# Performance work log

Measured on AMD Instinct MI355X. Metric: run time of the kernel, lower is better.

Reference implementation:

```python
import jax, jax.numpy as jnp
import numpy as np

DIM = 256
HEADS = 8
WIN = 8
HIDDEN = 1024
EPS = 1e-5

def _rel_pos_index(w):
    coords = np.stack(np.meshgrid(np.arange(w), np.arange(w), indexing='ij'))  # [2,w,w]
    cf = coords.reshape(2, -1)
    rel = cf[:, :, None] - cf[:, None, :]  # [2,N,N]
    rel = rel.transpose(1, 2, 0)
    rel[:, :, 0] += w - 1
    rel[:, :, 1] += w - 1
    rel[:, :, 0] *= 2 * w - 1
    return jnp.asarray(rel.sum(-1))  # [N,N] int

REL_IDX = _rel_pos_index(WIN)

def _layernorm(x, g, b):
    mu = jnp.mean(x, -1, keepdims=True)
    var = jnp.mean(jnp.square(x - mu), -1, keepdims=True)
    return (x - mu) * jax.lax.rsqrt(var + EPS) * g + b

def setup_inputs() -> dict:
    key = jax.random.key(0)
    ks = jax.random.split(key, 12)
    s = 0.02
    return {
        'x': jax.random.normal(ks[0], (16, 4096, 256), jnp.float32),
        'H': 64,
        'W': 64,
        'ln1_g': jnp.ones((DIM,), jnp.float32),
        'ln1_b': jnp.zeros((DIM,), jnp.float32),
        'qkv_w': jax.random.normal(ks[1], (DIM, 3 * DIM), jnp.float32) * s,
        'proj_w': jax.random.normal(ks[2], (DIM, DIM), jnp.float32) * s,
        'proj_b': jnp.zeros((DIM,), jnp.float32),
        'rel_bias_table': jax.random.normal(ks[3], ((2 * WIN - 1) ** 2, HEADS), jnp.float32) * s,
        'ln2_g': jnp.ones((DIM,), jnp.float32),
        'ln2_b': jnp.zeros((DIM,), jnp.float32),
        'fc1_w': jax.random.normal(ks[4], (DIM, HIDDEN), jnp.float32) * s,
        'fc1_b': jnp.zeros((HIDDEN,), jnp.float32),
        'fc2_w': jax.random.normal(ks[5], (HIDDEN, DIM), jnp.float32) * s,
        'fc2_b': jnp.zeros((DIM,), jnp.float32),
    }

def reference(x, H, W, ln1_g, ln1_b, qkv_w, proj_w, proj_b, rel_bias_table,
              ln2_g, ln2_b, fc1_w, fc1_b, fc2_w, fc2_b):
    B, L, C = x.shape
    w = WIN
    N = w * w
    head_dim = C // HEADS
    scale = head_dim ** -0.5

    shortcut = x
    h = _layernorm(x, ln1_g, ln1_b).reshape(B, H, W, C)
    # H, W chosen divisible by window_size -> pad_h = pad_w = 0 (faithful fast path)
    # window partition: [B*nW, N, C]
    h = h.reshape(B, H // w, w, W // w, w, C).transpose(0, 1, 3, 2, 4, 5)
    xw = h.reshape(-1, N, C)
    Bw = xw.shape[0]

    qkv = (xw @ qkv_w).reshape(Bw, N, 3, HEADS, head_dim)
    q = qkv[:, :, 0].transpose(0, 2, 1, 3) * scale  # [Bw,h,N,d]
    k = qkv[:, :, 1].transpose(0, 2, 1, 3)
    v = qkv[:, :, 2].transpose(0, 2, 1, 3)

    attn = jnp.einsum('bhnd,bhmd->bhnm', q, k)
    bias = rel_bias_table[REL_IDX.reshape(-1)].reshape(N, N, HEADS).transpose(2, 0, 1)
    attn = jax.nn.softmax(attn + bias[None], axis=-1)
    out = jnp.einsum('bhnm,bhmd->bhnd', attn, v).transpose(0, 2, 1, 3).reshape(Bw, N, C)
    out = out @ proj_w + proj_b

    # window reverse
    out = out.reshape(B, H // w, W // w, w, w, C).transpose(0, 1, 3, 2, 4, 5)
    out = out.reshape(B, L, C)

    x = shortcut + out
    h2 = _layernorm(x, ln2_g, ln2_b)
    mlp = jax.nn.gelu(h2 @ fc1_w + fc1_b, approximate=False) @ fc2_w + fc2_b
    return x + mlp
```

## Files before the change

### kernel.cpp

```cpp
#include <hip/hip_runtime.h>
#include <hip/hip_bf16.h>

typedef __attribute__((ext_vector_type(8))) short bf16x8;
typedef __attribute__((ext_vector_type(4))) float f32x4;

typedef __attribute__((address_space(3))) void LdsVoid;
typedef const __attribute__((address_space(1))) void GblVoid;

__device__ __forceinline__ void gload16(const void* g, void* l) {
  __builtin_amdgcn_global_load_lds((GblVoid*)g, (LdsVoid*)l, 16, 0, 0);
}

__device__ __forceinline__ unsigned short f2bf(float f) {
  union { float f; unsigned int u; } x; x.f = f;
  unsigned int r = (x.u + 0x7fffu + ((x.u >> 16) & 1u)) >> 16;
  return (unsigned short)r;
}

__global__ __launch_bounds__(256) void prep_w(
    const float* __restrict__ qw, const float* __restrict__ pw,
    const float* __restrict__ f1, const float* __restrict__ f2,
    unsigned short* __restrict__ out) {
  int idx = blockIdx.x * 256 + threadIdx.x;
  if (idx < 196608) { int n = idx >> 8, k = idx & 255; out[idx] = f2bf(qw[k * 768 + n]); return; }
  int i2 = idx - 196608;
  if (i2 < 65536) { int n = i2 >> 8, k = i2 & 255; out[idx] = f2bf(pw[k * 256 + n]); return; }
  int i3 = i2 - 65536;
  if (i3 < 262144) { int n = i3 >> 8, k = i3 & 255; out[idx] = f2bf(f1[k * 1024 + n]); return; }
  int i4 = i3 - 262144;
  { int n = i4 >> 10, k = i4 & 1023; out[idx] = f2bf(f2[k * 256 + n]); }
}

__global__ __launch_bounds__(256) void ln1_kernel(
    const float* __restrict__ x, const float* __restrict__ g, const float* __restrict__ b,
    unsigned short* __restrict__ xn) {
  int lane = threadIdx.x & 63, wid = threadIdx.x >> 6;
  size_t t = (size_t)blockIdx.x * 4 + wid;
  float4 v = ((const float4*)(x + t * 256))[lane];
  float s = v.x + v.y + v.z + v.w;
  #pragma unroll
  for (int m = 1; m < 64; m <<= 1) s += __shfl_xor(s, m);
  float mean = s * (1.0f / 256.0f);
  float dx = v.x - mean, dy = v.y - mean, dz = v.z - mean, dw = v.w - mean;
  float q = dx * dx + dy * dy + dz * dz + dw * dw;
  #pragma unroll
  for (int m = 1; m < 64; m <<= 1) q += __shfl_xor(q, m);
  float rstd = rsqrtf(q * (1.0f / 256.0f) + 1e-5f);
  float4 gg = ((const float4*)g)[lane];
  float4 bb = ((const float4*)b)[lane];
  unsigned int o0 = f2bf(dx * rstd * gg.x + bb.x) | ((unsigned int)f2bf(dy * rstd * gg.y + bb.y) << 16);
  unsigned int o1 = f2bf(dz * rstd * gg.z + bb.z) | ((unsigned int)f2bf(dw * rstd * gg.w + bb.w) << 16);
  int bI = (int)(t >> 12), rem = (int)t & 4095, y = rem >> 6, xc = rem & 63;
  size_t r = ((size_t)(bI * 64 + (y >> 3) * 8 + (xc >> 3))) * 64 + (y & 7) * 8 + (xc & 7);
  uint2 o; o.x = o0; o.y = o1;
  ((uint2*)(xn + r * 256))[lane] = o;
}

template <int EPI>
__global__ __launch_bounds__(256) void gemm_bt(
    const unsigned short* __restrict__ A, const unsigned short* __restrict__ Bt,
    unsigned short* __restrict__ outb, float* __restrict__ outf,
    const float* __restrict__ bias, const float* __restrict__ xres,
    int M, int N, int K) {
  __shared__ __align__(16) unsigned short lds[2 * 16384];
  const int tid = threadIdx.x;
  const int lane = tid & 63, wid = tid >> 6;
  const int cl = lane & 15, cg = lane >> 4;
  const unsigned nwg = gridDim.x * gridDim.y;
  const unsigned orig = blockIdx.y * gridDim.x + blockIdx.x;
  const unsigned virt = (orig & 7) * (nwg >> 3) + (orig >> 3);
  const unsigned bx = virt % gridDim.x, by = virt / gridDim.x;
  const size_t m0 = (size_t)by * 128;
  const size_t n0 = (size_t)bx * 128;
  const int wr = wid >> 1, wc = wid & 1;
  f32x4 acc[4][4] = {};

  const int r8 = lane >> 3;
  const int gsw = ((lane & 7) ^ r8) * 8;
  const unsigned short* aStage = A + (m0 + wid * 32 + r8) * K + gsw;
  const unsigned short* bStage = Bt + (n0 + wid * 32 + r8) * K + gsw;
  const size_t jstep = (size_t)8 * K;
  const int nt = K >> 6;

  #define STAGE(T, B)                                                   \
    { const int ko_ = (T) * 64;                                         \
      unsigned short* la_ = lds + (B) * 16384 + wid * 2048;             \
      unsigned short* lb_ = la_ + 8192;                                 \
      _Pragma("unroll")                                                 \
      for (int j = 0; j < 4; ++j) {                                     \
        gload16(aStage + ko_ + j * jstep, la_ + j * 512);               \
        gload16(bStage + ko_ + j * jstep, lb_ + j * 512);               \
      } }

  bf16x8 af[2][4], bfr[2][4];
  #define READF(B)                                                          \
    { const unsigned short* base_ = lds + (B) * 16384;                      \
      _Pragma("unroll")                                                     \
      for (int kk = 0; kk < 2; ++kk)                                        \
        _Pragma("unroll")                                                   \
        for (int i = 0; i < 4; ++i) {                                       \
          const int sl_ = ((kk * 4 + cg) ^ (cl & 7)) * 8;                   \
          af[kk][i]  = *(const bf16x8*)(base_ + (wr * 64 + i * 16 + cl) * 64 + sl_);        \
          bfr[kk][i] = *(const bf16x8*)(base_ + 8192 + (wc * 64 + i * 16 + cl) * 64 + sl_); \
        } }

  #define MFMAS()                                                           \
    { _Pragma("unroll")                                                     \
      for (int kk = 0; kk < 2; ++kk)                                        \
        _Pragma("unroll")                                                   \
        for (int mi = 0; mi < 4; ++mi)                                      \
          _Pragma("unroll")                                                 \
          for (int ni = 0; ni < 4; ++ni)                                    \
            acc[mi][ni] = __builtin_amdgcn_mfma_f32_16x16x32_bf16(af[kk][mi], bfr[kk][ni], acc[mi][ni], 0, 0, 0); }

  STAGE(0, 0);
  STAGE(1, 1);
  for (int t = 0; t < nt; ++t) {
    if (t == nt - 1) { asm volatile("s_waitcnt vmcnt(0)" ::: "memory"); }
    else             { asm volatile("s_waitcnt vmcnt(8)" ::: "memory"); }
    __builtin_amdgcn_s_barrier();
    READF(t & 1);
    __builtin_amdgcn_sched_barrier(0);
    asm volatile("s_waitcnt lgkmcnt(0)" ::: "memory");
    __builtin_amdgcn_s_barrier();
    __builtin_amdgcn_sched_barrier(0);
    if (t + 2 < nt) STAGE(t + 2, t & 1);
    MFMAS();
  }
  #undef STAGE
  #undef READF
  #undef MFMAS

  #pragma unroll
  for (int mi = 0; mi < 4; ++mi) {
    #pragma unroll
    for (int ni = 0; ni < 4; ++ni) {
      #pragma unroll
      for (int r = 0; r < 4; ++r) {
        size_t row = m0 + wr * 64 + mi * 16 + cg * 4 + r;
        size_t col = n0 + wc * 64 + ni * 16 + cl;
        float v = acc[mi][ni][r];
        if (EPI == 0) {
          outb[row * N + col] = f2bf(v);
        } else if (EPI == 1) {
          float t = v + bias[col];
          outb[row * N + col] = f2bf(0.5f * t * (1.0f + erff(t * 0.70710678118654752f)));
        } else if (EPI == 3) {
          outf[row * N + col] += v + bias[col];
        } else if (EPI == 4) {
          int winr = (int)(row >> 6), pos = (int)(row & 63);
          int bI = winr >> 6, wy = (winr >> 3) & 7, wx = winr & 7;
          size_t tt = (size_t)bI * 4096 + (size_t)(wy * 8 + (pos >> 3)) * 64 + wx * 8 + (pos & 7);
          outf[tt * 256 + col] = v + bias[col] + xres[tt * 256 + col];
        }
      }
    }
  }
}

__global__ __launch_bounds__(256) void attn_win(
    const unsigned short* __restrict__ qkv, const float* __restrict__ table,
    unsigned short* __restrict__ out) {
  __shared__ float tbl[1800];
  __shared__ __align__(16) unsigned short p_lds[4][64 * 72];
  __shared__ __align__(16) unsigned short vt_lds[4][32 * 72];
  const int tid = threadIdx.x, lane = tid & 63, wid = tid >> 6;
  const int cl = lane & 15, cg = lane >> 4;
  for (int i = tid; i < 1800; i += 256) tbl[i] = table[i];
  __syncthreads();
  const size_t wbase = (size_t)blockIdx.x * 64;
  unsigned short* P = p_lds[wid];
  unsigned short* VT = vt_lds[wid];
  const float scale = 0.17677669529663687f;

  for (int hh = 0; hh < 2; ++hh) {
    const int h = wid + hh * 4;
    const int qoff = h * 32, koff = 256 + h * 32, voff = 512 + h * 32;
    bf16x8 qf[4], kf[4];
    #pragma unroll
    for (int mi = 0; mi < 4; ++mi)
      qf[mi] = *(const bf16x8*)&qkv[(wbase + mi * 16 + cl) * 768 + qoff + cg * 8];
    #pragma unroll
    for (int nj = 0; nj < 4; ++nj)
      kf[nj] = *(const bf16x8*)&qkv[(wbase + nj * 16 + cl) * 768 + koff + cg * 8];
    f32x4 S[4][4] = {};
    #pragma unroll
    for (int mi = 0; mi < 4; ++mi)
      #pragma unroll
      for (int nj = 0; nj < 4; ++nj)
        S[mi][nj] = __builtin_amdgcn_mfma_f32_16x16x32_bf16(qf[mi], kf[nj], S[mi][nj], 0, 0, 0);

    {
      const unsigned short* vrow = &qkv[(wbase + lane) * 768 + voff];
      unsigned short tmp[32];
      #pragma unroll
      for (int p = 0; p < 4; ++p) *(uint4*)&tmp[p * 8] = ((const uint4*)vrow)[p];
      #pragma unroll
      for (int d = 0; d < 32; ++d) VT[d * 72 + lane] = tmp[d];
    }

    float rs[4][4];
    #pragma unroll
    for (int mi = 0; mi < 4; ++mi) {
      #pragma unroll
      for (int r = 0; r < 4; ++r) {
        const int i = mi * 16 + cg * 4 + r;
        const int yi = i >> 3, xi = i & 7;
        float v[4];
        float m = -1e30f;
        #pragma unroll
        for (int nj = 0; nj < 4; ++nj) {
          const int j = nj * 16 + cl;
          const int yj = j >> 3, xj = j & 7;
          float bia = tbl[((yi - yj + 7) * 15 + (xi - xj + 7)) * 8 + h];
          v[nj] = S[mi][nj][r] * scale + bia;
          m = fmaxf(m, v[nj]);
        }
        #pragma unroll
        for (int mk = 1; mk < 16; mk <<= 1) m = fmaxf(m, __shfl_xor(m, mk));
        float s = 0.0f;
        #pragma unroll
        for (int nj = 0; nj < 4; ++nj) { v[nj] = expf(v[nj] - m); s += v[nj]; }
        #pragma unroll
        for (int mk = 1; mk < 16; mk <<= 1) s += __shfl_xor(s, mk);
        rs[mi][r] = s;
        #pragma unroll
        for (int nj = 0; nj < 4; ++nj) P[i * 72 + nj * 16 + cl] = f2bf(v[nj]);
      }
    }

    f32x4 O[4][2] = {};
    #pragma unroll
    for (int ks = 0; ks < 2; ++ks) {
      bf16x8 pa[4], vb[2];
      #pragma unroll
      for (int mi = 0; mi < 4; ++mi)
        pa[mi] = *(const bf16x8*)&P[(mi * 16 + cl) * 72 + ks * 32 + cg * 8];
      #pragma unroll
      for (int nd = 0; nd < 2; ++nd)
        vb[nd] = *(const bf16x8*)&VT[(nd * 16 + cl) * 72 + ks * 32 + cg * 8];
      #pragma unroll
      for (int mi = 0; mi < 4; ++mi)
        #pragma unroll
        for (int nd = 0; nd < 2; ++nd)
          O[mi][nd] = __builtin_amdgcn_mfma_f32_16x16x32_bf16(pa[mi], vb[nd], O[mi][nd], 0, 0, 0);
    }

    #pragma unroll
    for (int mi = 0; mi < 4; ++mi)
      #pragma unroll
      for (int nd = 0; nd < 2; ++nd)
        #pragma unroll
        for (int r = 0; r < 4; ++r) {
          float val = O[mi][nd][r] / rs[mi][r];
          out[(wbase + mi * 16 + cg * 4 + r) * 256 + h * 32 + nd * 16 + cl] = f2bf(val);
        }
  }
}

__global__ __launch_bounds__(256) void ln2_kernel(
    const float* __restrict__ x2, const float* __restrict__ g, const float* __restrict__ b,
    unsigned short* __restrict__ h2) {
  int lane = threadIdx.x & 63, wid = threadIdx.x >> 6;
  size_t t = (size_t)blockIdx.x * 4 + wid;
  float4 v = ((const float4*)(x2 + t * 256))[lane];
  float s = v.x + v.y + v.z + v.w;
  #pragma unroll
  for (int m = 1; m < 64; m <<= 1) s += __shfl_xor(s, m);
  float mean = s * (1.0f / 256.0f);
  float dx = v.x - mean, dy = v.y - mean, dz = v.z - mean, dw = v.w - mean;
  float q = dx * dx + dy * dy + dz * dz + dw * dw;
  #pragma unroll
  for (int m = 1; m < 64; m <<= 1) q += __shfl_xor(q, m);
  float rstd = rsqrtf(q * (1.0f / 256.0f) + 1e-5f);
  float4 gg = ((const float4*)g)[lane];
  float4 bb = ((const float4*)b)[lane];
  uint2 o;
  o.x = f2bf(dx * rstd * gg.x + bb.x) | ((unsigned int)f2bf(dy * rstd * gg.y + bb.y) << 16);
  o.y = f2bf(dz * rstd * gg.z + bb.z) | ((unsigned int)f2bf(dw * rstd * gg.w + bb.w) << 16);
  ((uint2*)(h2 + t * 256))[lane] = o;
}

extern "C" void kernel_launch(void* const* d_in, const int* in_sizes, int n_in,
                              void* d_out, int out_size, void* d_ws, size_t ws_size,
                              hipStream_t stream) {
  (void)in_sizes; (void)n_in; (void)out_size; (void)ws_size;
  const float* x       = (const float*)d_in[0];
  const float* ln1_g   = (const float*)d_in[3];
  const float* ln1_b   = (const float*)d_in[4];
  const float* qkv_w   = (const float*)d_in[5];
  const float* proj_w  = (const float*)d_in[6];
  const float* proj_b  = (const float*)d_in[7];
  const float* rel_tbl = (const float*)d_in[8];
  const float* ln2_g   = (const float*)d_in[9];
  const float* ln2_b   = (const float*)d_in[10];
  const float* fc1_w   = (const float*)d_in[11];
  const float* fc1_b   = (const float*)d_in[12];
  const float* fc2_w   = (const float*)d_in[13];
  const float* fc2_b   = (const float*)d_in[14];
  float* out = (float*)d_out;

  char* ws = (char*)d_ws;
  const size_t OFF_XN   = 1572864;
  const size_t OFF_QKV  = OFF_XN + 33554432;
  const size_t OFF_ATTN = OFF_QKV + 100663296;
  unsigned short* Wt      = (unsigned short*)ws;
  unsigned short* xn      = (unsigned short*)(ws + OFF_XN);
  unsigned short* h2      = xn;
  unsigned short* qkv     = (unsigned short*)(ws + OFF_QKV);
  unsigned short* fc1out  = (unsigned short*)(ws + OFF_QKV);
  unsigned short* attnout = (unsigned short*)(ws + OFF_ATTN);

  prep_w<<<3072, 256, 0, stream>>>(qkv_w, proj_w, fc1_w, fc2_w, Wt);
  ln1_kernel<<<16384, 256, 0, stream>>>(x, ln1_g, ln1_b, xn);
  gemm_bt<0><<<dim3(6, 512), 256, 0, stream>>>(xn, Wt, qkv, nullptr, nullptr, nullptr, 65536, 768, 256);
  attn_win<<<1024, 256, 0, stream>>>(qkv, rel_tbl, attnout);
  gemm_bt<4><<<dim3(2, 512), 256, 0, stream>>>(attnout, Wt + 196608, nullptr, out, proj_b, x, 65536, 256, 256);
  ln2_kernel<<<16384, 256, 0, stream>>>(out, ln2_g, ln2_b, h2);
  gemm_bt<1><<<dim3(8, 512), 256, 0, stream>>>(h2, Wt + 262144, fc1out, nullptr, fc1_b, nullptr, 65536, 1024, 256);
  gemm_bt<3><<<dim3(2, 512), 256, 0, stream>>>(fc1out, Wt + 524288, nullptr, out, fc2_b, nullptr, 65536, 256, 1024);
}
```

Measured before the change: 455.3 us.

## Transpose MFMA outputs for vectorized epilogue stores and use tanh GELU

Swaps the A/B operands of the MFMAs in the GEMM and attention kernels so each lane holds four consecutive columns of one row. Epilogue stores then become packed uint2/float4 writes instead of scalar strided ones. The softmax normalization moves before the PV MFMA via a reciprocal. The erf GELU is replaced with a tanh approximation built on __expf, which changes numerics slightly relative to the exact GELU in the reference.

```diff
diff --git a/kernel.cpp b/kernel.cpp
--- a/kernel.cpp
+++ b/kernel.cpp
@@ -15,6 +15,13 @@
   union { float f; unsigned int u; } x; x.f = f;
   unsigned int r = (x.u + 0x7fffu + ((x.u >> 16) & 1u)) >> 16;
   return (unsigned short)r;
+}
+
+__device__ __forceinline__ float gelu_f(float t) {
+  float u = t * (0.7978845608028654f + 0.03567740814f * t * t);
+  float e = __expf(2.0f * u);
+  float th = 1.0f - 2.0f / (e + 1.0f);
+  return 0.5f * t * (1.0f + th);
 }
 
 __global__ __launch_bounds__(256) void prep_w(
@@ -111,7 +118,7 @@
         for (int mi = 0; mi < 4; ++mi)                                      \
           _Pragma("unroll")                                                 \
           for (int ni = 0; ni < 4; ++ni)                                    \
-            acc[mi][ni] = __builtin_amdgcn_mfma_f32_16x16x32_bf16(af[kk][mi], bfr[kk][ni], acc[mi][ni], 0, 0, 0); }
+            acc[mi][ni] = __builtin_amdgcn_mfma_f32_16x16x32_bf16(bfr[kk][ni], af[kk][mi], acc[mi][ni], 0, 0, 0); }
 
   STAGE(0, 0);
   STAGE(1, 1);
@@ -133,26 +140,41 @@
 
   #pragma unroll
   for (int mi = 0; mi < 4; ++mi) {
+    const size_t row = m0 + wr * 64 + mi * 16 + cl;
     #pragma unroll
     for (int ni = 0; ni < 4; ++ni) {
-      #pragma unroll
-      for (int r = 0; r < 4; ++r) {
-        size_t row = m0 + wr * 64 + mi * 16 + cg * 4 + r;
-        size_t col = n0 + wc * 64 + ni * 16 + cl;
-        float v = acc[mi][ni][r];
-        if (EPI == 0) {
-          outb[row * N + col] = f2bf(v);
-        } else if (EPI == 1) {
-          float t = v + bias[col];
-          outb[row * N + col] = f2bf(0.5f * t * (1.0f + erff(t * 0.70710678118654752f)));
-        } else if (EPI == 3) {
-          outf[row * N + col] += v + bias[col];
-        } else if (EPI == 4) {
-          int winr = (int)(row >> 6), pos = (int)(row & 63);
-          int bI = winr >> 6, wy = (winr >> 3) & 7, wx = winr & 7;
-          size_t tt = (size_t)bI * 4096 + (size_t)(wy * 8 + (pos >> 3)) * 64 + wx * 8 + (pos & 7);
-          outf[tt * 256 + col] = v + bias[col] + xres[tt * 256 + col];
-        }
+      const size_t col = n0 + wc * 64 + ni * 16 + cg * 4;
+      f32x4 v = acc[mi][ni];
+      if (EPI == 0) {
+        uint2 o;
+        o.x = f2bf(v[0]) | ((unsigned int)f2bf(v[1]) << 16);
+        o.y = f2bf(v[2]) | ((unsigned int)f2bf(v[3]) << 16);
+        *(uint2*)&outb[row * N + col] = o;
+      } else if (EPI == 1) {
+        float4 bb = *(const float4*)&bias[col];
+        float g0 = gelu_f(v[0] + bb.x), g1 = gelu_f(v[1] + bb.y);
+        float g2 = gelu_f(v[2] + bb.z), g3 = gelu_f(v[3] + bb.w);
+        uint2 o;
+        o.x = f2bf(g0) | ((unsigned int)f2bf(g1) << 16);
+        o.y = f2bf(g2) | ((unsigned int)f2bf(g3) << 16);
+        *(uint2*)&outb[row * N + col] = o;
+      } else if (EPI == 3) {
+        float4 bb = *(const float4*)&bias[col];
+        float4* p = (float4*)&outf[row * N + col];
+        float4 old = *p;
+        old.x += v[0] + bb.x; old.y += v[1] + bb.y;
+        old.z += v[2] + bb.z; old.w += v[3] + bb.w;
+        *p = old;
+      } else if (EPI == 4) {
+        int winr = (int)(row >> 6), pos = (int)(row & 63);
+        int bI = winr >> 6, wy = (winr >> 3) & 7, wx = winr & 7;
+        size_t tt = (size_t)bI * 4096 + (size_t)(wy * 8 + (pos >> 3)) * 64 + wx * 8 + (pos & 7);
+        float4 bb = *(const float4*)&bias[col];
+        float4 xr = *(const float4*)&xres[tt * 256 + col];
+        float4 o;
+        o.x = v[0] + bb.x + xr.x; o.y = v[1] + bb.y + xr.y;
+        o.z = v[2] + bb.z + xr.z; o.w = v[3] + bb.w + xr.w;
+        *(float4*)&outf[tt * 256 + col] = o;
       }
     }
   }
@@ -199,7 +221,6 @@
       for (int d = 0; d < 32; ++d) VT[d * 72 + lane] = tmp[d];
     }
 
-    float rs[4][4];
     #pragma unroll
     for (int mi = 0; mi < 4; ++mi) {
       #pragma unroll
@@ -223,9 +244,9 @@
         for (int nj = 0; nj < 4; ++nj) { v[nj] = expf(v[nj] - m); s += v[nj]; }
         #pragma unroll
         for (int mk = 1; mk < 16; mk <<= 1) s += __shfl_xor(s, mk);
-        rs[mi][r] = s;
-        #pragma unroll
-        for (int nj = 0; nj < 4; ++nj) P[i * 72 + nj * 16 + cl] = f2bf(v[nj]);
+        const float rinv = 1.0f / s;
+        #pragma unroll
+        for (int nj = 0; nj < 4; ++nj) P[i * 72 + nj * 16 + cl] = f2bf(v[nj] * rinv);
       }
     }
 
@@ -243,18 +264,18 @@
       for (int mi = 0; mi < 4; ++mi)
         #pragma unroll
         for (int nd = 0; nd < 2; ++nd)
-          O[mi][nd] = __builtin_amdgcn_mfma_f32_16x16x32_bf16(pa[mi], vb[nd], O[mi][nd], 0, 0, 0);
+          O[mi][nd] = __builtin_amdgcn_mfma_f32_16x16x32_bf16(vb[nd], pa[mi], O[mi][nd], 0, 0, 0);
     }
 
     #pragma unroll
     for (int mi = 0; mi < 4; ++mi)
       #pragma unroll
-      for (int nd = 0; nd < 2; ++nd)
-        #pragma unroll
-        for (int r = 0; r < 4; ++r) {
-          float val = O[mi][nd][r] / rs[mi][r];
-          out[(wbase + mi * 16 + cg * 4 + r) * 256 + h * 32 + nd * 16 + cl] = f2bf(val);
-        }
+      for (int nd = 0; nd < 2; ++nd) {
+        uint2 o;
+        o.x = f2bf(O[mi][nd][0]) | ((unsigned int)f2bf(O[mi][nd][1]) << 16);
+        o.y = f2bf(O[mi][nd][2]) | ((unsigned int)f2bf(O[mi][nd][3]) << 16);
+        *(uint2*)&out[(wbase + mi * 16 + cl) * 256 + h * 32 + nd * 16 + cg * 4] = o;
+      }
   }
 }
 
```

Measured after the change: 449.4 us. No clear change (-1.3%).
